# Kernel tuning notes

Measured on AMD Instinct MI355X. Metric: run time of the kernel, lower is better.

## Reference

```python
import jax, jax.numpy as jnp
import numpy as np

B, S, H, V, C = 32, 512, 256, 50000, 5
NUM_LAYERS, WINDOW = 2, 2


def setup_inputs() -> dict:
    key = jax.random.key(0)
    ks = jax.random.split(key, 24)
    std = 0.1  # matches nn.init.normal_(p, 0, 0.1)
    n = lambda k, shp: jax.random.normal(k, shp, dtype=jnp.float32) * std
    u = lambda k, shp: -0.05 + jax.random.uniform(k, shp, dtype=jnp.float32) * 0.1
    return {
        "input_sentences": jax.random.randint(ks[0], (B, S), 0, V),
        "sentences_length": jax.random.randint(ks[1], (B,), 1, S),
        "hh0": u(ks[2], (B, S, H)),
        "cs0": u(ks[3], (B, S, H)),
        "embed": n(ks[4], (V, H)),
        # stacked word-gate weights, gate order: i, l, r, f, s, output, u
        "W_lr": n(ks[5], (7, H, 2 * H)),
        "W_c": n(ks[6], (7, H, H)),
        "W_x": n(ks[7], (7, H, H)),
        "W_g": n(ks[8], (7, H, H)),
        "gate_bias": n(ks[9], (7, H)),
        # sentence-state gates
        "W_fg_g": n(ks[10], (H, H)),
        "W_fg_h": n(ks[11], (H, H)),
        "W_fgi_g": n(ks[12], (H, H)),
        "W_fgi_h": n(ks[13], (H, H)),
        "W_og_g": n(ks[14], (H, H)),
        "W_og_h": n(ks[15], (H, H)),
        "b_fg": n(ks[16], (H,)),
        "b_fgi": n(ks[17], (H,)),
        # output head
        "W1": n(ks[18], (H, 2 * H)),
        "b1": n(ks[19], (H,)),
        "Wout": n(ks[20], (C, H)),
        "bout": n(ks[21], (C,)),
    }


def _before_sum(x, window):
    # sum of right-shifted (zero-padded at front) copies, shifts 1..window
    out = jnp.zeros_like(x)
    for s in range(1, window + 1):
        out = out + jnp.pad(x[:, :-s], ((0, 0), (s, 0), (0, 0)))
    return out


def _after_sum(x, window):
    out = jnp.zeros_like(x)
    for s in range(1, window + 1):
        out = out + jnp.pad(x[:, s:], ((0, 0), (0, s), (0, 0)))
    return out


def _slstm_step(hh, cs, sv, scs, wv, W_lr, W_c, W_x, W_g, gate_bias,
                W_fg_g, W_fg_h, W_fgi_g, W_fgi_h, W_og_g, W_og_h, b_fg, b_fgi):
    avg_hh = hh.mean(axis=1)                                   # [B,H]
    f_hat_g = jax.nn.sigmoid(sv @ W_fg_g.T + avg_hh @ W_fg_h.T + b_fg)
    # NOTE: original code (faithfully) uses output_gate_bias here, not output_gate_g_bias
    og_g = jax.nn.sigmoid(sv @ W_og_g.T + avg_hh @ W_og_h.T + gate_bias[5])
    f_hat_g_i = jax.nn.sigmoid((sv @ W_fgi_g.T)[:, None] + hh @ W_fgi_h.T + b_fgi)
    scores = jax.nn.softmax(f_hat_g_i, axis=2)                 # over hidden dim
    new_scs = jax.nn.softmax(f_hat_g, axis=1) * scs + (scores * cs).sum(axis=1)
    new_sv = og_g * jnp.tanh(new_scs)

    hb = _before_sum(hh, WINDOW)
    ha = _after_sum(hh, WINDOW)
    cb = _before_sum(cs, WINDOW)
    ca = _after_sum(cs, WINDOW)
    ba = jnp.concatenate([hb, ha], axis=-1)                    # [B,S,2H]

    # all 7 gate pre-activations at once: [B,S,7,H]
    pre = (jnp.einsum('bsk,ghk->bsgh', ba, W_lr)
           + jnp.einsum('bsk,ghk->bsgh', hh, W_c)
           + jnp.einsum('bsk,ghk->bsgh', wv, W_x)
           + (jnp.einsum('bk,ghk->bgh', new_sv, W_g) + gate_bias)[:, None])

    g5 = jax.nn.sigmoid(pre[..., :5, :])                       # i,l,r,f,s
    b_, s_ = g5.shape[:2]
    # joint softmax over the concatenated 5*H gate vector (as in torch cat+softmax)
    g5 = jax.nn.softmax(g5.reshape(b_, s_, -1), axis=-1).reshape(b_, s_, 5, -1)
    i_t, l_t, r_t, f_t, s_t = (g5[..., k, :] for k in range(5))
    og = jax.nn.sigmoid(pre[..., 5, :])
    u_g = jnp.tanh(pre[..., 6, :])

    new_cs = l_t * cb + f_t * cs + r_t * ca + s_t * scs[:, None] + i_t * u_g
    new_hh = og * jnp.tanh(new_cs)
    return new_hh, new_cs, new_sv, new_scs


def reference(input_sentences, sentences_length, hh0, cs0, embed,
              W_lr, W_c, W_x, W_g, gate_bias,
              W_fg_g, W_fg_h, W_fgi_g, W_fgi_h, W_og_g, W_og_h, b_fg, b_fgi,
              W1, b1, Wout, bout):
    wv = embed[input_sentences]                                # [B,S,H]
    hh, cs = hh0, cs0
    sv, scs = hh0.mean(axis=1), cs0.mean(axis=1)
    for _ in range(NUM_LAYERS):
        hh, cs, sv, scs = _slstm_step(hh, cs, sv, scs, wv,
                                      W_lr, W_c, W_x, W_g, gate_bias,
                                      W_fg_g, W_fg_h, W_fgi_g, W_fgi_h,
                                      W_og_g, W_og_h, b_fg, b_fgi)
    avg_hh = hh.mean(axis=1)
    conc = jnp.concatenate([avg_hh, sv], axis=1) @ W1.T + b1
    fc = conc @ Wout.T + bout
    return jax.nn.log_softmax(fc, axis=1), sv
```

## Files before the change

kernel.cpp:

```cpp
#include <hip/hip_runtime.h>
#include <stdint.h>
#include <math.h>

#define B_   32
#define S_   512
#define H_   256
#define M_   (B_*S_)
#define KBIG 1024
#define NB   1792
#define C_   5

typedef __bf16 bf16;
typedef __bf16 bf16x4 __attribute__((ext_vector_type(4)));
typedef __bf16 bf16x8 __attribute__((ext_vector_type(8)));
typedef float  floatx4 __attribute__((ext_vector_type(4)));

__device__ __forceinline__ float sigm(float x){ return 1.f/(1.f+expf(-x)); }

__device__ __forceinline__ void gl16(const bf16* g, bf16* l){
    __builtin_amdgcn_global_load_lds(
        (const __attribute__((address_space(1))) unsigned int*)g,
        (__attribute__((address_space(3))) unsigned int*)l, 16, 0, 0);
}

__global__ void wcomb_k(const float* __restrict__ Wlr, const float* __restrict__ Wc,
                        const float* __restrict__ Wx, bf16* __restrict__ WT){
    int n = blockIdx.x;
    int g = n >> 8, h = n & 255;
    int k4 = threadIdx.x * 4;
    const float* src;
    if (k4 < 512)      src = Wlr + ((size_t)(g*256 + h))*512 + k4;
    else if (k4 < 768) src = Wc  + ((size_t)(g*256 + h))*256 + (k4 - 512);
    else               src = Wx  + ((size_t)(g*256 + h))*256 + (k4 - 768);
    float4 v = *(const float4*)src;
    bf16 o[4] = {(bf16)v.x,(bf16)v.y,(bf16)v.z,(bf16)v.w};
    *(uint2*)&WT[(size_t)n*KBIG + k4] = *(uint2*)o;
}

__global__ void cvtw_k(const float* __restrict__ a, bf16* __restrict__ o){
    int i4 = (blockIdx.x*256 + threadIdx.x)*4;
    float4 v = *(const float4*)(a + i4);
    bf16 t[4] = {(bf16)v.x,(bf16)v.y,(bf16)v.z,(bf16)v.w};
    *(uint2*)(o + i4) = *(uint2*)t;
}

__global__ void gather_k(const int* __restrict__ idx, const float* __restrict__ embed,
                         bf16* __restrict__ wv){
    int i4 = (blockIdx.x*256 + threadIdx.x)*4;
    int m = i4 >> 8, h = i4 & 255;
    float4 v = *(const float4*)(embed + (size_t)idx[m]*H_ + h);
    bf16 o[4] = {(bf16)v.x,(bf16)v.y,(bf16)v.z,(bf16)v.w};
    *(uint2*)(wv + (size_t)m*H_ + h) = *(uint2*)o;
}

__global__ void mean1_k(const float* __restrict__ x, float* __restrict__ part){
    int b = blockIdx.x, c = blockIdx.y, h = threadIdx.x;
    const float* p = x + ((size_t)b*S_ + c*32)*H_ + h;
    float s = 0.f;
    #pragma unroll 8
    for (int t=0;t<32;t++) s += p[(size_t)t*H_];
    part[((size_t)b*16 + c)*H_ + h] = s;
}
__global__ void mean2_k(const float* __restrict__ part, float* __restrict__ out){
    int b = blockIdx.x, h = threadIdx.x;
    float s = 0.f;
    #pragma unroll
    for (int c=0;c<16;c++) s += part[((size_t)b*16 + c)*H_ + h];
    out[b*H_ + h] = s * (1.f/512.f);
}

__global__ void buildx_k(const float* __restrict__ hh, const bf16* __restrict__ wv,
                         bf16* __restrict__ X){
    int m = blockIdx.x, tid = threadIdx.x;
    int seg = tid >> 6, li = tid & 63;
    int s = m & (S_-1);
    int h0 = li*4;
    size_t base = (size_t)m*H_ + h0;
    bf16* xr = X + (size_t)m*KBIG + seg*H_ + h0;
    const float4 z = {0.f,0.f,0.f,0.f};
    if (seg == 3){
        *(uint2*)xr = *(const uint2*)&wv[base];
        return;
    }
    float4 v;
    if (seg == 0){
        float4 a = (s>=1) ? *(const float4*)&hh[base - H_]   : z;
        float4 b = (s>=2) ? *(const float4*)&hh[base - 2*H_] : z;
        v.x=a.x+b.x; v.y=a.y+b.y; v.z=a.z+b.z; v.w=a.w+b.w;
    } else if (seg == 1){
        float4 a = (s<=S_-2) ? *(const float4*)&hh[base + H_]   : z;
        float4 b = (s<=S_-3) ? *(const float4*)&hh[base + 2*H_] : z;
        v.x=a.x+b.x; v.y=a.y+b.y; v.z=a.z+b.z; v.w=a.w+b.w;
    } else {
        v = *(const float4*)&hh[base];
    }
    bf16 o[4] = {(bf16)v.x,(bf16)v.y,(bf16)v.z,(bf16)v.w};
    *(uint2*)xr = *(uint2*)o;
}

__global__ void mv5_k(const float* __restrict__ sv, const float* __restrict__ avg,
    const float* __restrict__ Wfg_g, const float* __restrict__ Wfg_h,
    const float* __restrict__ Wog_g, const float* __restrict__ Wog_h,
    const float* __restrict__ Wfgi_g, float* __restrict__ res){
    int j = blockIdx.x, b = blockIdx.y, h = threadIdx.x;
    const float* vec = (j==1 || j==3) ? avg + b*H_ : sv + b*H_;
    const float* W   = (j==0)?Wfg_g:(j==1)?Wfg_h:(j==2)?Wog_g:(j==3)?Wog_h:Wfgi_g;
    __shared__ float v[H_];
    v[h] = vec[h]; __syncthreads();
    const float* w = W + (size_t)h*H_;
    float d = 0.f;
    for (int k=0;k<H_;k++) d += v[k]*w[k];
    res[((size_t)b*5 + j)*H_ + h] = d;
}
__global__ void comb_k(const float* __restrict__ res, const float* __restrict__ b_fg,
                       const float* __restrict__ gbias, const float* __restrict__ b_fgi,
                       float* __restrict__ fhg, float* __restrict__ ogg,
                       float* __restrict__ svg){
    int b = blockIdx.x, h = threadIdx.x;
    const float* r = res + (size_t)b*5*H_;
    fhg[b*H_+h] = sigm(r[h] + r[H_+h] + b_fg[h]);
    ogg[b*H_+h] = sigm(r[2*H_+h] + r[3*H_+h] + gbias[5*H_+h]);
    svg[b*H_+h] = r[4*H_+h] + b_fgi[h];
}

template<int EPI>
__global__ __launch_bounds__(256)
void mgemm_k(const bf16* __restrict__ A, const bf16* __restrict__ BT,
             bf16* __restrict__ C, const float* __restrict__ gt,
             int Kdim, int lda, int ldb, int ldc){
    __shared__ alignas(16) bf16 lsA[128*32];
    __shared__ alignas(16) bf16 lsB[128*32];
    int tid  = threadIdx.x;
    int m0 = blockIdx.y * 128, n0 = blockIdx.x * 128;
    int wave = tid >> 6, lane = tid & 63;
    int wm = (wave & 1) * 64, wn = (wave >> 1) * 64;
    int lrow = lane & 15, quad = lane >> 4;

    floatx4 zero = {0.f,0.f,0.f,0.f};
    floatx4 acc[4][4];
    #pragma unroll
    for (int i=0;i<4;i++)
        #pragma unroll
        for (int j=0;j<4;j++) acc[i][j] = zero;

    int srow = tid >> 2;
    int scol = (tid & 3) * 8;
    const bf16* Abase = A  + (size_t)(m0 + srow)*lda + scol;
    const bf16* Bbase = BT + (size_t)(n0 + srow)*ldb + scol;
    bf16* dA0 = &lsA[srow*32 + scol];
    bf16* dA1 = &lsA[(64+srow)*32 + scol];
    bf16* dB0 = &lsB[srow*32 + scol];
    bf16* dB1 = &lsB[(64+srow)*32 + scol];

    for (int k0 = 0; k0 < Kdim; k0 += 32){
        __syncthreads();
        gl16(Abase + k0,                     dA0);
        gl16(Abase + (size_t)64*lda + k0,    dA1);
        gl16(Bbase + k0,                     dB0);
        gl16(Bbase + (size_t)64*ldb + k0,    dB1);
        __syncthreads();
        bf16x8 af[4], bfr[4];
        #pragma unroll
        for (int mi=0;mi<4;mi++) af[mi]  = *(const bf16x8*)&lsA[(wm+mi*16+lrow)*32 + quad*8];
        #pragma unroll
        for (int ni=0;ni<4;ni++) bfr[ni] = *(const bf16x8*)&lsB[(wn+ni*16+lrow)*32 + quad*8];
        #pragma unroll
        for (int mi=0;mi<4;mi++)
            #pragma unroll
            for (int ni=0;ni<4;ni++)
                acc[mi][ni] = __builtin_amdgcn_mfma_f32_16x16x32_bf16(af[mi], bfr[ni], acc[mi][ni], 0, 0, 0);
    }

    #pragma unroll
    for (int mi=0;mi<4;mi++)
        #pragma unroll
        for (int ni=0;ni<4;ni++){
            int row = m0 + wm + mi*16 + quad*4;
            int col = n0 + wn + ni*16 + lrow;
            #pragma unroll
            for (int r=0;r<4;r++){
                float v = acc[mi][ni][r];
                if (EPI) v += gt[(size_t)((row+r)>>9)*NB + col];
                C[(size_t)(row+r)*ldc + col] = (bf16)v;
            }
        }
}

template<int EPI>
__device__ __forceinline__ void mmq(floatx4 (&acc)[8][4], bf16x8 (&af)[4][2], bf16x8 (&bfr)[2][2],
                                    int MH, int NH){
    #pragma unroll
    for (int mi2=0;mi2<4;mi2++)
        #pragma unroll
        for (int ni2=0;ni2<2;ni2++)
            #pragma unroll
            for (int kk=0;kk<2;kk++)
                acc[MH*4+mi2][NH*2+ni2] = __builtin_amdgcn_mfma_f32_16x16x32_bf16(
                    af[mi2][kk], bfr[ni2][kk], acc[MH*4+mi2][NH*2+ni2], 0, 0, 0);
}

template<int EPI>
__global__ __launch_bounds__(512, 2)
void mgemm256_k(const bf16* __restrict__ A, const bf16* __restrict__ BT,
                bf16* __restrict__ C, const float* __restrict__ gt,
                int Kdim, int lda, int ldb, int ldc, int nbx){
    __shared__ alignas(16) bf16 lsA[2][256*64];
    __shared__ alignas(16) bf16 lsB[2][256*64];
    const int tid  = threadIdx.x;
    const int lane = tid & 63;
    const int wave = tid >> 6;
    const int wm = wave >> 2;
    const int wn = wave & 3;
    const int lrow = lane & 15, quad = lane >> 4;

    const int nwg = gridDim.x;
    const int cpx = nwg >> 3;
    const int w   = (blockIdx.x & 7)*cpx + (blockIdx.x >> 3);
    const int mb  = w / nbx, nb = w - mb*nbx;
    const int m0 = mb * 256, n0 = nb * 256;

    const int srow = tid >> 3;
    const int scol = ((tid & 7) ^ (srow & 7)) * 8;
    const bf16* Ab = A  + (size_t)(m0 + srow)*lda + scol;
    const bf16* Bb = BT + (size_t)(n0 + srow)*ldb + scol;
    const int NT = Kdim >> 6;

    floatx4 zero = {0.f,0.f,0.f,0.f};
    floatx4 acc[8][4];
    #pragma unroll
    for (int i=0;i<8;i++)
        #pragma unroll
        for (int j=0;j<4;j++) acc[i][j] = zero;
    bf16x8 af[4][2], bfr[2][2];

#define SA_(bu,r,kt) gl16(Ab + (size_t)(r)*64*lda + (size_t)(kt)*64, &lsA[bu][(r)*4096 + tid*8])
#define SB_(bu,r,kt) gl16(Bb + (size_t)(r)*64*ldb + (size_t)(kt)*64, &lsB[bu][(r)*4096 + tid*8])
#define RA_(bu,MH,mi2,kk) (*(const bf16x8*)&lsA[bu][(wm*128 + (MH)*64 + (mi2)*16 + lrow)*64 + ((((kk)*4+quad) ^ (lrow&7))*8)])
#define RB_(bu,NH,ni2,kk) (*(const bf16x8*)&lsB[bu][(wn*64  + (NH)*32 + (ni2)*16 + lrow)*64 + ((((kk)*4+quad) ^ (lrow&7))*8)])

    SB_(0,0,0); SB_(0,1,0); SB_(0,2,0); SB_(0,3,0);
    SA_(0,0,0); SA_(0,2,0); SA_(0,1,0); SA_(0,3,0);
    asm volatile("s_waitcnt vmcnt(2)" ::: "memory");
    __builtin_amdgcn_s_barrier();

    for (int kt = 0; kt < NT; ++kt){
        const int cur = kt & 1, nxt = cur ^ 1;
        const bool st = (kt + 1 < NT);
        const int k1 = kt + 1;

        if (st){
            SB_(nxt,0,k1); SB_(nxt,1,k1); SB_(nxt,2,k1); SB_(nxt,3,k1);
            SA_(nxt,0,k1); SA_(nxt,2,k1); SA_(nxt,1,k1); SA_(nxt,3,k1);
        }

        #pragma unroll
        for (int mi2=0;mi2<4;mi2++){ af[mi2][0] = RA_(cur,0,mi2,0); af[mi2][1] = RA_(cur,0,mi2,1); }
        #pragma unroll
        for (int ni2=0;ni2<2;ni2++){ bfr[ni2][0] = RB_(cur,0,ni2,0); bfr[ni2][1] = RB_(cur,0,ni2,1); }
        __builtin_amdgcn_s_barrier();
        __builtin_amdgcn_s_setprio(1);
        mmq<EPI>(acc, af, bfr, 0, 0);
        __builtin_amdgcn_s_setprio(0);
        __builtin_amdgcn_s_barrier();

        #pragma unroll
        for (int ni2=0;ni2<2;ni2++){ bfr[ni2][0] = RB_(cur,1,ni2,0); bfr[ni2][1] = RB_(cur,1,ni2,1); }
        __builtin_amdgcn_s_barrier();
        __builtin_amdgcn_s_setprio(1);
        mmq<EPI>(acc, af, bfr, 0, 1);
        __builtin_amdgcn_s_setprio(0);
        if (st) asm volatile("s_waitcnt vmcnt(8)" ::: "memory");
        else    asm volatile("s_waitcnt vmcnt(0)" ::: "memory");
        __builtin_amdgcn_s_barrier();

        #pragma unroll
        for (int mi2=0;mi2<4;mi2++){ af[mi2][0] = RA_(cur,1,mi2,0); af[mi2][1] = RA_(cur,1,mi2,1); }
        __builtin_amdgcn_s_barrier();
        __builtin_amdgcn_s_setprio(1);
        mmq<EPI>(acc, af, bfr, 1, 1);
        __builtin_amdgcn_s_setprio(0);
        __builtin_amdgcn_s_barrier();

        #pragma unroll
        for (int ni2=0;ni2<2;ni2++){ bfr[ni2][0] = RB_(cur,0,ni2,0); bfr[ni2][1] = RB_(cur,0,ni2,1); }
        __builtin_amdgcn_s_barrier();
        __builtin_amdgcn_s_setprio(1);
        mmq<EPI>(acc, af, bfr, 1, 0);
        __builtin_amdgcn_s_setprio(0);
        if (st) asm volatile("s_waitcnt vmcnt(2)" ::: "memory");
        __builtin_amdgcn_s_barrier();
    }
#undef SA_
#undef SB_
#undef RA_
#undef RB_

    float gtv[4] = {0.f,0.f,0.f,0.f};
    if (EPI){
        const int b = m0 >> 9;
        #pragma unroll
        for (int ni=0;ni<4;ni++)
            gtv[ni] = gt[(size_t)b*NB + n0 + wn*64 + ni*16 + lrow];
    }
    #pragma unroll
    for (int mi=0;mi<8;mi++)
        #pragma unroll
        for (int ni=0;ni<4;ni++){
            int row = m0 + wm*128 + mi*16 + quad*4;
            int col = n0 + wn*64  + ni*16 + lrow;
            #pragma unroll
            for (int r=0;r<4;r++){
                float v = acc[mi][ni][r];
                if (EPI) v += gtv[ni];
                C[(size_t)(row+r)*ldc + col] = (bf16)v;
            }
        }
}

__global__ void scorep_k(const bf16* __restrict__ fgih, const float* __restrict__ svg,
                         const float* __restrict__ cs, float* __restrict__ part){
    int chunk = blockIdx.x, b = blockIdx.y;
    int tid = threadIdx.x, wave = tid >> 6, lane = tid & 63;
    __shared__ float acc4[4][256];
    float sw[4], acc[4] = {0.f,0.f,0.f,0.f};
    #pragma unroll
    for (int j=0;j<4;j++) sw[j] = svg[b*H_ + lane + 64*j];
    for (int t=wave; t<16; t+=4){
        int m = b*S_ + chunk*16 + t;
        const bf16* fr = fgih + (size_t)m*H_;
        float e[4], loc = 0.f;
        #pragma unroll
        for (int j=0;j<4;j++){ e[j] = expf(sigm(sw[j] + (float)fr[lane+64*j])); loc += e[j]; }
        #pragma unroll
        for (int off=32; off; off>>=1) loc += __shfl_xor(loc, off, 64);
        float inv = 1.f/loc;
        const float* cr = cs + (size_t)m*H_;
        #pragma unroll
        for (int j=0;j<4;j++) acc[j] += e[j]*inv*cr[lane+64*j];
    }
    #pragma unroll
    for (int j=0;j<4;j++) acc4[wave][lane+64*j] = acc[j];
    __syncthreads();
    part[((size_t)b*32 + chunk)*H_ + tid] =
        acc4[0][tid] + acc4[1][tid] + acc4[2][tid] + acc4[3][tid];
}

__global__ void newscs_k(const float* __restrict__ part, const float* __restrict__ fhg,
                         const float* __restrict__ ogg, const float* __restrict__ scs_in,
                         float* __restrict__ scs_out, float* __restrict__ sv_out){
    int b = blockIdx.x, h = threadIdx.x;
    __shared__ float r[256];
    float dot = 0.f;
    #pragma unroll 8
    for (int c=0;c<32;c++) dot += part[((size_t)b*32+c)*H_ + h];
    float e = expf(fhg[b*H_+h]);
    r[h] = e; __syncthreads();
    for (int off=128; off; off>>=1){ if (h<off) r[h] += r[h+off]; __syncthreads(); }
    float ns = (e / r[0]) * scs_in[b*H_+h] + dot;
    scs_out[b*H_+h] = ns;
    sv_out[b*H_+h]  = ogg[b*H_+h] * tanhf(ns);
}

__global__ void gterm_k(const float* __restrict__ svn, const float* __restrict__ Wg,
                        const float* __restrict__ gbias, float* __restrict__ gt){
    int g = blockIdx.x, b = blockIdx.y, h = threadIdx.x;
    __shared__ float s[H_];
    s[h] = svn[b*H_+h]; __syncthreads();
    const float* w = Wg + ((size_t)g*H_ + h)*H_;
    float d = 0.f;
    for (int k=0;k<H_;k++) d += s[k]*w[k];
    gt[(size_t)b*NB + g*H_ + h] = d + gbias[g*H_+h];
}

__global__ void gates_k(const bf16* __restrict__ pre, const float* __restrict__ cs_in,
                        const float* __restrict__ scs_in,
                        float* __restrict__ hh_out, float* __restrict__ cs_out){
    int tid = threadIdx.x, wave = tid >> 6, lane = tid & 63;
    int m = blockIdx.x*4 + wave;
    int b = m >> 9, s = m & (S_-1);
    const bf16* row = pre + (size_t)m*NB;
    int h0 = lane*4;
    float pv[7][4];
    #pragma unroll
    for (int g=0; g<7; ++g){
        bf16x4 t = *(const bf16x4*)&row[g*H_ + h0];
        #pragma unroll
        for (int j=0;j<4;j++) pv[g][j] = (float)t[j];
    }
    float ex[5][4], og[4], u[4];
    float loc = 0.f;
    #pragma unroll
    for (int g=0; g<5; ++g)
        #pragma unroll
        for (int j=0;j<4;j++){ float e = expf(sigm(pv[g][j])); ex[g][j] = e; loc += e; }
    #pragma unroll
    for (int j=0;j<4;j++){ og[j] = sigm(pv[5][j]); u[j] = tanhf(pv[6][j]); }
    #pragma unroll
    for (int off=32; off; off>>=1) loc += __shfl_xor(loc, off, 64);
    float inv = 1.f / loc;

    size_t i0 = (size_t)m*H_ + h0;
    const float4 z = {0.f,0.f,0.f,0.f};
    float4 c0  = *(const float4*)&cs_in[i0];
    float4 cm1 = (s>=1)    ? *(const float4*)&cs_in[i0 - H_]   : z;
    float4 cm2 = (s>=2)    ? *(const float4*)&cs_in[i0 - 2*H_] : z;
    float4 cp1 = (s<=S_-2) ? *(const float4*)&cs_in[i0 + H_]   : z;
    float4 cp2 = (s<=S_-3) ? *(const float4*)&cs_in[i0 + 2*H_] : z;
    float4 sc  = *(const float4*)&scs_in[(size_t)b*H_ + h0];
    float4 nc4, nh4;
    #pragma unroll
    for (int j=0;j<4;j++){
        float cb = ((const float*)&cm1)[j] + ((const float*)&cm2)[j];
        float ca = ((const float*)&cp1)[j] + ((const float*)&cp2)[j];
        float nc = ex[1][j]*inv*cb + ex[3][j]*inv*((const float*)&c0)[j] + ex[2][j]*inv*ca
                 + ex[4][j]*inv*((const float*)&sc)[j] + ex[0][j]*inv*u[j];
        ((float*)&nc4)[j] = nc;
        ((float*)&nh4)[j] = og[j] * tanhf(nc);
    }
    *(float4*)&cs_out[i0] = nc4;
    *(float4*)&hh_out[i0] = nh4;
}

__global__ void head_k(const float* __restrict__ avgh, const float* __restrict__ sv,
                       const float* __restrict__ W1, const float* __restrict__ b1,
                       const float* __restrict__ Wout, const float* __restrict__ bout,
                       float* __restrict__ out){
    int b = blockIdx.x, t = threadIdx.x;
    __shared__ float conc[H_];
    __shared__ float fc[8];
    const float* wr = W1 + (size_t)t*512;
    float d = b1[t];
    for (int k=0;k<H_;k++) d += avgh[b*H_+k]*wr[k];
    for (int k=0;k<H_;k++) d += sv[b*H_+k]*wr[256+k];
    conc[t] = d;
    __syncthreads();
    if (t < C_){
        const float* wo = Wout + (size_t)t*H_;
        float s = bout[t];
        for (int i=0;i<H_;i++) s += conc[i]*wo[i];
        fc[t] = s;
    }
    __syncthreads();
    if (t == 0){
        float mx = fc[0];
        for (int c=1;c<C_;c++) mx = fmaxf(mx, fc[c]);
        float se = 0.f;
        for (int c=0;c<C_;c++) se += expf(fc[c]-mx);
        float lse = mx + logf(se);
        for (int c=0;c<C_;c++) out[b*C_+c] = fc[c]-lse;
    }
    out[B_*C_ + b*H_ + t] = sv[b*H_+t];
}

extern "C" void kernel_launch(void* const* d_in, const int* in_sizes, int n_in,
                              void* d_out, int out_size, void* d_ws, size_t ws_size,
                              hipStream_t stream){
    const int*   idx    = (const int*)d_in[0];
    const float* hh0    = (const float*)d_in[2];
    const float* cs0    = (const float*)d_in[3];
    const float* embed  = (const float*)d_in[4];
    const float* Wlr    = (const float*)d_in[5];
    const float* Wc     = (const float*)d_in[6];
    const float* Wx     = (const float*)d_in[7];
    const float* Wg     = (const float*)d_in[8];
    const float* gbias  = (const float*)d_in[9];
    const float* Wfg_g  = (const float*)d_in[10];
    const float* Wfg_h  = (const float*)d_in[11];
    const float* Wfgi_g = (const float*)d_in[12];
    const float* Wfgi_h = (const float*)d_in[13];
    const float* Wog_g  = (const float*)d_in[14];
    const float* Wog_h  = (const float*)d_in[15];
    const float* b_fg   = (const float*)d_in[16];
    const float* b_fgi  = (const float*)d_in[17];
    const float* W1     = (const float*)d_in[18];
    const float* b1     = (const float*)d_in[19];
    const float* Wout   = (const float*)d_in[20];
    const float* bout   = (const float*)d_in[21];

    uint8_t* p = (uint8_t*)d_ws;
    auto alloc = [&](size_t bytes)->void*{ void* r=(void*)p; p += (bytes + 255) & ~(size_t)255; return r; };
    bf16*  WT    = (bf16*)alloc((size_t)NB*KBIG*2);
    bf16*  WfgiT = (bf16*)alloc((size_t)H_*H_*2);
    bf16*  X     = (bf16*)alloc((size_t)M_*KBIG*2);
    bf16*  wv    = (bf16*)alloc((size_t)M_*H_*2);
    bf16*  pre   = (bf16*)alloc((size_t)M_*NB*2);
    bf16*  fgih  = (bf16*)alloc((size_t)M_*H_*2);
    float* hhA = (float*)alloc((size_t)M_*H_*4);
    float* csA = (float*)alloc((size_t)M_*H_*4);
    float* hhB = (float*)alloc((size_t)M_*H_*4);
    float* csB = (float*)alloc((size_t)M_*H_*4);
    float* mpart= (float*)alloc((size_t)B_*16*H_*4);
    float* part = (float*)alloc((size_t)B_*32*H_*4);
    float* res5 = (float*)alloc((size_t)B_*5*H_*4);
    float* avgh = (float*)alloc(B_*H_*4);
    float* fhg  = (float*)alloc(B_*H_*4);
    float* ogg  = (float*)alloc(B_*H_*4);
    float* svg  = (float*)alloc(B_*H_*4);
    float* svP0 = (float*)alloc(B_*H_*4);
    float* svP1 = (float*)alloc(B_*H_*4);
    float* scP0 = (float*)alloc(B_*H_*4);
    float* scP1 = (float*)alloc(B_*H_*4);
    float* gt   = (float*)alloc((size_t)B_*NB*4);

    wcomb_k <<<NB,          256, 0, stream>>>(Wlr, Wc, Wx, WT);
    cvtw_k  <<<(H_*H_)/1024,256, 0, stream>>>(Wfgi_h, WfgiT);
    gather_k<<<(M_*H_)/1024,256, 0, stream>>>(idx, embed, wv);
    mean1_k <<<dim3(B_,16), 256, 0, stream>>>(hh0, mpart);
    mean2_k <<<B_,          256, 0, stream>>>(mpart, svP0);
    mean1_k <<<dim3(B_,16), 256, 0, stream>>>(cs0, mpart);
    mean2_k <<<B_,          256, 0, stream>>>(mpart, scP0);

    const float *hin = hh0, *cin = cs0;
    float *hout = hhA, *cout = csA;
    float *svin = svP0, *scin = scP0, *svout = svP1, *scout = scP1;

    for (int l=0; l<2; ++l){
        const float* avgp;
        if (l == 0){
            avgp = svin;
        } else {
            mean1_k<<<dim3(B_,16), 256, 0, stream>>>(hin, mpart);
            mean2_k<<<B_,          256, 0, stream>>>(mpart, avgh);
            avgp = avgh;
        }
        mv5_k   <<<dim3(5,B_), 256, 0, stream>>>(svin, avgp, Wfg_g, Wfg_h, Wog_g,
                                                 Wog_h, Wfgi_g, res5);
        comb_k  <<<B_, 256, 0, stream>>>(res5, b_fg, gbias, b_fgi, fhg, ogg, svg);
        buildx_k<<<M_, 256, 0, stream>>>(hin, wv, X);
        mgemm_k<0><<<dim3(2,128), 256, 0, stream>>>(X+512, WfgiT, fgih, nullptr,
                                                    H_, KBIG, H_, H_);
        scorep_k<<<dim3(32,B_), 256, 0, stream>>>(fgih, svg, cin, part);
        newscs_k<<<B_, 256, 0, stream>>>(part, fhg, ogg, scin, scout, svout);
        gterm_k <<<dim3(7,B_), 256, 0, stream>>>(svout, Wg, gbias, gt);
        mgemm256_k<1><<<448, 512, 0, stream>>>(X, WT, pre, gt,
                                               KBIG, KBIG, KBIG, NB, 7);
        gates_k <<<M_/4, 256, 0, stream>>>(pre, cin, scin, hout, cout);
        hin = hout; cin = cout;
        hout = (l==0) ? hhB : hhA;
        cout = (l==0) ? csB : csA;
        float* q;
        q = svin; svin = svout; svout = q;
        q = scin; scin = scout; scout = q;
    }
    mean1_k<<<dim3(B_,16), 256, 0, stream>>>(hin, mpart);
    mean2_k<<<B_,          256, 0, stream>>>(mpart, avgh);
    head_k <<<B_, 256, 0, stream>>>(avgh, svin, W1, b1, Wout, bout, (float*)d_out);
}
```

Measured before the change: 554.0 us.

## Fold fgi GEMM into main gate GEMM and move gate bias to gates kernel

Appends the W_fgi_h weights, zero-padded to K=1024, as 256 extra output columns of the big combined weight matrix. One 256x256-tile GEMM launch (512 blocks) now produces both the gate preactivations and the fgi projection, which removes the separate small GEMM kernel and its launch. Because the sentence-gate term now depends on scorep results computed after this GEMM, the bias and gt addition moves from the GEMM epilogue into gates_k. The cost is a wider pre buffer with stride 2048 and some wasted MACs on the zero-padded K. The main loop also reorders the global-to-LDS prefetch issues, splitting them across the four MFMA phases with separate B-fragment registers and adjusted vmcnt waits.

```diff
diff --git a/kernel.cpp b/kernel.cpp
--- a/kernel.cpp
+++ b/kernel.cpp
@@ -8,6 +8,7 @@
 #define M_   (B_*S_)
 #define KBIG 1024
 #define NB   1792
+#define NB2  2048
 #define C_   5
 
 typedef __bf16 bf16;
@@ -24,24 +25,25 @@
 }
 
 __global__ void wcomb_k(const float* __restrict__ Wlr, const float* __restrict__ Wc,
-                        const float* __restrict__ Wx, bf16* __restrict__ WT){
+                        const float* __restrict__ Wx, const float* __restrict__ Wfgi,
+                        bf16* __restrict__ WT){
     int n = blockIdx.x;
-    int g = n >> 8, h = n & 255;
     int k4 = threadIdx.x * 4;
-    const float* src;
-    if (k4 < 512)      src = Wlr + ((size_t)(g*256 + h))*512 + k4;
-    else if (k4 < 768) src = Wc  + ((size_t)(g*256 + h))*256 + (k4 - 512);
-    else               src = Wx  + ((size_t)(g*256 + h))*256 + (k4 - 768);
-    float4 v = *(const float4*)src;
+    float4 v;
+    if (n < NB){
+        int g = n >> 8, h = n & 255;
+        const float* src;
+        if (k4 < 512)      src = Wlr + ((size_t)(g*256 + h))*512 + k4;
+        else if (k4 < 768) src = Wc  + ((size_t)(g*256 + h))*256 + (k4 - 512);
+        else               src = Wx  + ((size_t)(g*256 + h))*256 + (k4 - 768);
+        v = *(const float4*)src;
+    } else {
+        int h = n - NB;
+        if (k4 >= 512 && k4 < 768) v = *(const float4*)(Wfgi + (size_t)h*H_ + (k4 - 512));
+        else { v.x=0.f; v.y=0.f; v.z=0.f; v.w=0.f; }
+    }
     bf16 o[4] = {(bf16)v.x,(bf16)v.y,(bf16)v.z,(bf16)v.w};
     *(uint2*)&WT[(size_t)n*KBIG + k4] = *(uint2*)o;
-}
-
-__global__ void cvtw_k(const float* __restrict__ a, bf16* __restrict__ o){
-    int i4 = (blockIdx.x*256 + threadIdx.x)*4;
-    float4 v = *(const float4*)(a + i4);
-    bf16 t[4] = {(bf16)v.x,(bf16)v.y,(bf16)v.z,(bf16)v.w};
-    *(uint2*)(o + i4) = *(uint2*)t;
 }
 
 __global__ void gather_k(const int* __restrict__ idx, const float* __restrict__ embed,
@@ -123,70 +125,6 @@
     svg[b*H_+h] = r[4*H_+h] + b_fgi[h];
 }
 
-template<int EPI>
-__global__ __launch_bounds__(256)
-void mgemm_k(const bf16* __restrict__ A, const bf16* __restrict__ BT,
-             bf16* __restrict__ C, const float* __restrict__ gt,
-             int Kdim, int lda, int ldb, int ldc){
-    __shared__ alignas(16) bf16 lsA[128*32];
-    __shared__ alignas(16) bf16 lsB[128*32];
-    int tid  = threadIdx.x;
-    int m0 = blockIdx.y * 128, n0 = blockIdx.x * 128;
-    int wave = tid >> 6, lane = tid & 63;
-    int wm = (wave & 1) * 64, wn = (wave >> 1) * 64;
-    int lrow = lane & 15, quad = lane >> 4;
-
-    floatx4 zero = {0.f,0.f,0.f,0.f};
-    floatx4 acc[4][4];
-    #pragma unroll
-    for (int i=0;i<4;i++)
-        #pragma unroll
-        for (int j=0;j<4;j++) acc[i][j] = zero;
-
-    int srow = tid >> 2;
-    int scol = (tid & 3) * 8;
-    const bf16* Abase = A  + (size_t)(m0 + srow)*lda + scol;
-    const bf16* Bbase = BT + (size_t)(n0 + srow)*ldb + scol;
-    bf16* dA0 = &lsA[srow*32 + scol];
-    bf16* dA1 = &lsA[(64+srow)*32 + scol];
-    bf16* dB0 = &lsB[srow*32 + scol];
-    bf16* dB1 = &lsB[(64+srow)*32 + scol];
-
-    for (int k0 = 0; k0 < Kdim; k0 += 32){
-        __syncthreads();
-        gl16(Abase + k0,                     dA0);
-        gl16(Abase + (size_t)64*lda + k0,    dA1);
-        gl16(Bbase + k0,                     dB0);
-        gl16(Bbase + (size_t)64*ldb + k0,    dB1);
-        __syncthreads();
-        bf16x8 af[4], bfr[4];
-        #pragma unroll
-        for (int mi=0;mi<4;mi++) af[mi]  = *(const bf16x8*)&lsA[(wm+mi*16+lrow)*32 + quad*8];
-        #pragma unroll
-        for (int ni=0;ni<4;ni++) bfr[ni] = *(const bf16x8*)&lsB[(wn+ni*16+lrow)*32 + quad*8];
-        #pragma unroll
-        for (int mi=0;mi<4;mi++)
-            #pragma unroll
-            for (int ni=0;ni<4;ni++)
-                acc[mi][ni] = __builtin_amdgcn_mfma_f32_16x16x32_bf16(af[mi], bfr[ni], acc[mi][ni], 0, 0, 0);
-    }
-
-    #pragma unroll
-    for (int mi=0;mi<4;mi++)
-        #pragma unroll
-        for (int ni=0;ni<4;ni++){
-            int row = m0 + wm + mi*16 + quad*4;
-            int col = n0 + wn + ni*16 + lrow;
-            #pragma unroll
-            for (int r=0;r<4;r++){
-                float v = acc[mi][ni][r];
-                if (EPI) v += gt[(size_t)((row+r)>>9)*NB + col];
-                C[(size_t)(row+r)*ldc + col] = (bf16)v;
-            }
-        }
-}
-
-template<int EPI>
 __device__ __forceinline__ void mmq(floatx4 (&acc)[8][4], bf16x8 (&af)[4][2], bf16x8 (&bfr)[2][2],
                                     int MH, int NH){
     #pragma unroll
@@ -199,11 +137,9 @@
                     af[mi2][kk], bfr[ni2][kk], acc[MH*4+mi2][NH*2+ni2], 0, 0, 0);
 }
 
-template<int EPI>
 __global__ __launch_bounds__(512, 2)
 void mgemm256_k(const bf16* __restrict__ A, const bf16* __restrict__ BT,
-                bf16* __restrict__ C, const float* __restrict__ gt,
-                int Kdim, int lda, int ldb, int ldc, int nbx){
+                bf16* __restrict__ C, int Kdim, int lda, int ldb, int ldc, int nbx){
     __shared__ alignas(16) bf16 lsA[2][256*64];
     __shared__ alignas(16) bf16 lsB[2][256*64];
     const int tid  = threadIdx.x;
@@ -213,8 +149,7 @@
     const int wn = wave & 3;
     const int lrow = lane & 15, quad = lane >> 4;
 
-    const int nwg = gridDim.x;
-    const int cpx = nwg >> 3;
+    const int cpx = gridDim.x >> 3;
     const int w   = (blockIdx.x & 7)*cpx + (blockIdx.x >> 3);
     const int mb  = w / nbx, nb = w - mb*nbx;
     const int m0 = mb * 256, n0 = nb * 256;
@@ -231,7 +166,7 @@
     for (int i=0;i<8;i++)
         #pragma unroll
         for (int j=0;j<4;j++) acc[i][j] = zero;
-    bf16x8 af[4][2], bfr[2][2];
+    bf16x8 af[4][2], bfrA[2][2], bfrB[2][2];
 
 #define SA_(bu,r,kt) gl16(Ab + (size_t)(r)*64*lda + (size_t)(kt)*64, &lsA[bu][(r)*4096 + tid*8])
 #define SB_(bu,r,kt) gl16(Bb + (size_t)(r)*64*ldb + (size_t)(kt)*64, &lsB[bu][(r)*4096 + tid*8])
@@ -248,44 +183,41 @@
         const bool st = (kt + 1 < NT);
         const int k1 = kt + 1;
 
-        if (st){
-            SB_(nxt,0,k1); SB_(nxt,1,k1); SB_(nxt,2,k1); SB_(nxt,3,k1);
-            SA_(nxt,0,k1); SA_(nxt,2,k1); SA_(nxt,1,k1); SA_(nxt,3,k1);
-        }
-
         #pragma unroll
         for (int mi2=0;mi2<4;mi2++){ af[mi2][0] = RA_(cur,0,mi2,0); af[mi2][1] = RA_(cur,0,mi2,1); }
         #pragma unroll
-        for (int ni2=0;ni2<2;ni2++){ bfr[ni2][0] = RB_(cur,0,ni2,0); bfr[ni2][1] = RB_(cur,0,ni2,1); }
+        for (int ni2=0;ni2<2;ni2++){ bfrA[ni2][0] = RB_(cur,0,ni2,0); bfrA[ni2][1] = RB_(cur,0,ni2,1); }
+        if (st){ SB_(nxt,0,k1); SB_(nxt,1,k1); }
         __builtin_amdgcn_s_barrier();
         __builtin_amdgcn_s_setprio(1);
-        mmq<EPI>(acc, af, bfr, 0, 0);
+        mmq(acc, af, bfrA, 0, 0);
         __builtin_amdgcn_s_setprio(0);
         __builtin_amdgcn_s_barrier();
 
         #pragma unroll
-        for (int ni2=0;ni2<2;ni2++){ bfr[ni2][0] = RB_(cur,1,ni2,0); bfr[ni2][1] = RB_(cur,1,ni2,1); }
+        for (int ni2=0;ni2<2;ni2++){ bfrB[ni2][0] = RB_(cur,1,ni2,0); bfrB[ni2][1] = RB_(cur,1,ni2,1); }
+        if (st){ SB_(nxt,2,k1); SB_(nxt,3,k1); }
         __builtin_amdgcn_s_barrier();
         __builtin_amdgcn_s_setprio(1);
-        mmq<EPI>(acc, af, bfr, 0, 1);
+        mmq(acc, af, bfrB, 0, 1);
         __builtin_amdgcn_s_setprio(0);
-        if (st) asm volatile("s_waitcnt vmcnt(8)" ::: "memory");
+        if (st) asm volatile("s_waitcnt vmcnt(4)" ::: "memory");
         else    asm volatile("s_waitcnt vmcnt(0)" ::: "memory");
         __builtin_amdgcn_s_barrier();
 
         #pragma unroll
         for (int mi2=0;mi2<4;mi2++){ af[mi2][0] = RA_(cur,1,mi2,0); af[mi2][1] = RA_(cur,1,mi2,1); }
+        if (st){ SA_(nxt,0,k1); SA_(nxt,2,k1); }
         __builtin_amdgcn_s_barrier();
         __builtin_amdgcn_s_setprio(1);
-        mmq<EPI>(acc, af, bfr, 1, 1);
+        mmq(acc, af, bfrB, 1, 1);
         __builtin_amdgcn_s_setprio(0);
         __builtin_amdgcn_s_barrier();
 
-        #pragma unroll
-        for (int ni2=0;ni2<2;ni2++){ bfr[ni2][0] = RB_(cur,0,ni2,0); bfr[ni2][1] = RB_(cur,0,ni2,1); }
+        if (st){ SA_(nxt,1,k1); SA_(nxt,3,k1); }
         __builtin_amdgcn_s_barrier();
         __builtin_amdgcn_s_setprio(1);
-        mmq<EPI>(acc, af, bfr, 1, 0);
+        mmq(acc, af, bfrA, 1, 0);
         __builtin_amdgcn_s_setprio(0);
         if (st) asm volatile("s_waitcnt vmcnt(2)" ::: "memory");
         __builtin_amdgcn_s_barrier();
@@ -295,13 +227,6 @@
 #undef RA_
 #undef RB_
 
-    float gtv[4] = {0.f,0.f,0.f,0.f};
-    if (EPI){
-        const int b = m0 >> 9;
-        #pragma unroll
-        for (int ni=0;ni<4;ni++)
-            gtv[ni] = gt[(size_t)b*NB + n0 + wn*64 + ni*16 + lrow];
-    }
     #pragma unroll
     for (int mi=0;mi<8;mi++)
         #pragma unroll
@@ -309,16 +234,13 @@
             int row = m0 + wm*128 + mi*16 + quad*4;
             int col = n0 + wn*64  + ni*16 + lrow;
             #pragma unroll
-            for (int r=0;r<4;r++){
-                float v = acc[mi][ni][r];
-                if (EPI) v += gtv[ni];
-                C[(size_t)(row+r)*ldc + col] = (bf16)v;
-            }
+            for (int r=0;r<4;r++)
+                C[(size_t)(row+r)*ldc + col] = (bf16)acc[mi][ni][r];
         }
 }
 
 __global__ void scorep_k(const bf16* __restrict__ fgih, const float* __restrict__ svg,
-                         const float* __restrict__ cs, float* __restrict__ part){
+                         const float* __restrict__ cs, float* __restrict__ part, int ldf){
     int chunk = blockIdx.x, b = blockIdx.y;
     int tid = threadIdx.x, wave = tid >> 6, lane = tid & 63;
     __shared__ float acc4[4][256];
@@ -327,7 +249,7 @@
     for (int j=0;j<4;j++) sw[j] = svg[b*H_ + lane + 64*j];
     for (int t=wave; t<16; t+=4){
         int m = b*S_ + chunk*16 + t;
-        const bf16* fr = fgih + (size_t)m*H_;
+        const bf16* fr = fgih + (size_t)m*ldf;
         float e[4], loc = 0.f;
         #pragma unroll
         for (int j=0;j<4;j++){ e[j] = expf(sigm(sw[j] + (float)fr[lane+64*j])); loc += e[j]; }
@@ -372,20 +294,23 @@
     gt[(size_t)b*NB + g*H_ + h] = d + gbias[g*H_+h];
 }
 
-__global__ void gates_k(const bf16* __restrict__ pre, const float* __restrict__ cs_in,
-                        const float* __restrict__ scs_in,
-                        float* __restrict__ hh_out, float* __restrict__ cs_out){
+__global__ void gates_k(const bf16* __restrict__ pre, const float* __restrict__ gt,
+                        const float* __restrict__ cs_in, const float* __restrict__ scs_in,
+                        float* __restrict__ hh_out, float* __restrict__ cs_out, int ldp){
     int tid = threadIdx.x, wave = tid >> 6, lane = tid & 63;
     int m = blockIdx.x*4 + wave;
     int b = m >> 9, s = m & (S_-1);
-    const bf16* row = pre + (size_t)m*NB;
+    const bf16* row = pre + (size_t)m*ldp;
     int h0 = lane*4;
     float pv[7][4];
     #pragma unroll
     for (int g=0; g<7; ++g){
         bf16x4 t = *(const bf16x4*)&row[g*H_ + h0];
-        #pragma unroll
-        for (int j=0;j<4;j++) pv[g][j] = (float)t[j];
+        float4 gq = *(const float4*)&gt[(size_t)b*NB + g*H_ + h0];
+        pv[g][0] = (float)t[0] + gq.x;
+        pv[g][1] = (float)t[1] + gq.y;
+        pv[g][2] = (float)t[2] + gq.z;
+        pv[g][3] = (float)t[3] + gq.w;
     }
     float ex[5][4], og[4], u[4];
     float loc = 0.f;
@@ -479,12 +404,10 @@
 
     uint8_t* p = (uint8_t*)d_ws;
     auto alloc = [&](size_t bytes)->void*{ void* r=(void*)p; p += (bytes + 255) & ~(size_t)255; return r; };
-    bf16*  WT    = (bf16*)alloc((size_t)NB*KBIG*2);
-    bf16*  WfgiT = (bf16*)alloc((size_t)H_*H_*2);
+    bf16*  WT    = (bf16*)alloc((size_t)NB2*KBIG*2);
     bf16*  X     = (bf16*)alloc((size_t)M_*KBIG*2);
     bf16*  wv    = (bf16*)alloc((size_t)M_*H_*2);
-    bf16*  pre   = (bf16*)alloc((size_t)M_*NB*2);
-    bf16*  fgih  = (bf16*)alloc((size_t)M_*H_*2);
+    bf16*  pre   = (bf16*)alloc((size_t)M_*NB2*2);
     float* hhA = (float*)alloc((size_t)M_*H_*4);
     float* csA = (float*)alloc((size_t)M_*H_*4);
     float* hhB = (float*)alloc((size_t)M_*H_*4);
@@ -502,8 +425,7 @@
     float* scP1 = (float*)alloc(B_*H_*4);
     float* gt   = (float*)alloc((size_t)B_*NB*4);
 
-    wcomb_k <<<NB,          256, 0, stream>>>(Wlr, Wc, Wx, WT);
-    cvtw_k  <<<(H_*H_)/1024,256, 0, stream>>>(Wfgi_h, WfgiT);
+    wcomb_k <<<NB2,         256, 0, stream>>>(Wlr, Wc, Wx, Wfgi_h, WT);
     gather_k<<<(M_*H_)/1024,256, 0, stream>>>(idx, embed, wv);
     mean1_k <<<dim3(B_,16), 256, 0, stream>>>(hh0, mpart);
     mean2_k <<<B_,          256, 0, stream>>>(mpart, svP0);
@@ -527,14 +449,11 @@
                                                  Wog_h, Wfgi_g, res5);
         comb_k  <<<B_, 256, 0, stream>>>(res5, b_fg, gbias, b_fgi, fhg, ogg, svg);
         buildx_k<<<M_, 256, 0, stream>>>(hin, wv, X);
-        mgemm_k<0><<<dim3(2,128), 256, 0, stream>>>(X+512, WfgiT, fgih, nullptr,
-                                                    H_, KBIG, H_, H_);
-        scorep_k<<<dim3(32,B_), 256, 0, stream>>>(fgih, svg, cin, part);
+        mgemm256_k<<<512, 512, 0, stream>>>(X, WT, pre, KBIG, KBIG, KBIG, NB2, 8);
+        scorep_k<<<dim3(32,B_), 256, 0, stream>>>(pre + NB, svg, cin, part, NB2);
         newscs_k<<<B_, 256, 0, stream>>>(part, fhg, ogg, scin, scout, svout);
         gterm_k <<<dim3(7,B_), 256, 0, stream>>>(svout, Wg, gbias, gt);
-        mgemm256_k<1><<<448, 512, 0, stream>>>(X, WT, pre, gt,
-                                               KBIG, KBIG, KBIG, NB, 7);
-        gates_k <<<M_/4, 256, 0, stream>>>(pre, cin, scin, hout, cout);
+        gates_k <<<M_/4, 256, 0, stream>>>(pre, gt, cin, scin, hout, cout, NB2);
         hin = hout; cin = cout;
         hout = (l==0) ? hhB : hhA;
         cout = (l==0) ? csB : csA;
```

Measured after the change: 516.5 us. 6.8% less time.
